# Optimization experiments

Measured on AMD Instinct MI355X. Metric: run time of the kernel, lower is better.

The kernel has to match this reference:

```python
import jax, jax.numpy as jnp
import numpy as np
import math

MSG_K = 256  # min(active_count, 256); with uniform(0,1) activations active_count >> 256
N_HEADS = 4
LN_EPS = 1e-5


def _mha(x, wi, bi, wo, bo):
    # torch nn.MultiheadAttention self-attention, batch_first=True
    B, K, D = x.shape
    H = N_HEADS
    hd = D // H
    qkv = x @ wi.T + bi                      # [B,K,3D]
    q, k, v = jnp.split(qkv, 3, axis=-1)
    def split_heads(t):
        return t.reshape(B, K, H, hd).transpose(0, 2, 1, 3)  # [B,H,K,hd]
    q, k, v = split_heads(q), split_heads(k), split_heads(v)
    scores = jnp.einsum('bhqd,bhkd->bhqk', q, k) * (1.0 / math.sqrt(hd))
    attn = jax.nn.softmax(scores, axis=-1)
    o = jnp.einsum('bhqk,bhkd->bhqd', attn, v)
    o = o.transpose(0, 2, 1, 3).reshape(B, K, D)
    return o @ wo.T + bo


def _layernorm(x, g, b):
    mu = jnp.mean(x, axis=-1, keepdims=True)
    var = jnp.mean((x - mu) ** 2, axis=-1, keepdims=True)
    return (x - mu) * jax.lax.rsqrt(var + LN_EPS) * g + b


def setup_inputs() -> dict:
    key = jax.random.key(0)
    ks = jax.random.split(key, 12)
    B, N, D = 32, 4096, 256
    s = 0.02
    return {
        'activation': jax.random.uniform(ks[0], (B, N), dtype=jnp.float32),
        'hidden_state': jax.random.normal(ks[1], (B, N, D), dtype=jnp.float32),
        'in_proj_w': jax.random.normal(ks[2], (3 * D, D), dtype=jnp.float32) * s,
        'in_proj_b': jnp.zeros((3 * D,), jnp.float32),
        'out_proj_w': jax.random.normal(ks[3], (D, D), dtype=jnp.float32) * s,
        'out_proj_b': jnp.zeros((D,), jnp.float32),
        'su_w1': jax.random.normal(ks[4], (D, 2 * D), dtype=jnp.float32) * s,
        'su_b1': jnp.zeros((D,), jnp.float32),
        'su_w2': jax.random.normal(ks[5], (D, D), dtype=jnp.float32) * s,
        'su_b2': jnp.zeros((D,), jnp.float32),
        'au_w1': jax.random.normal(ks[6], (D, 2 * D), dtype=jnp.float32) * s,
        'au_b1': jnp.zeros((D,), jnp.float32),
        'au_w2': jax.random.normal(ks[7], (1, D), dtype=jnp.float32) * s,
        'au_b2': jnp.zeros((1,), jnp.float32),
        'ln_g': jnp.ones((D,), jnp.float32),
        'ln_b': jnp.zeros((D,), jnp.float32),
        'sparsity_k': 256,
    }


def reference(activation, hidden_state, in_proj_w, in_proj_b, out_proj_w, out_proj_b,
              su_w1, su_b1, su_w2, su_b2, au_w1, au_b1, au_w2, au_b2, ln_g, ln_b,
              sparsity_k):
    B, N, D = hidden_state.shape
    b_idx = jnp.arange(B)[:, None]

    # ---- compute_messages: top-k gather -> sparse MHA -> scatter back ----
    topk_vals, topk_idx = jax.lax.top_k(activation, MSG_K)        # [B,K]
    active_states = jnp.take_along_axis(hidden_state, topk_idx[..., None], axis=1)  # [B,K,D]
    msg_sparse = _mha(active_states, in_proj_w, in_proj_b, out_proj_w, out_proj_b)
    msg_sparse = msg_sparse * topk_vals[..., None]
    messages = jnp.zeros((B, N, D), hidden_state.dtype).at[b_idx, topk_idx].set(msg_sparse)

    # ---- update_states: MLP on [old, messages] + LayerNorm ----
    combined = jnp.concatenate([hidden_state, messages], axis=-1)  # [B,N,2D]
    h = jax.nn.gelu(combined @ su_w1.T + su_b1, approximate=False)
    new_hidden = _layernorm(h @ su_w2.T + su_b2, ln_g, ln_b)

    # ---- update_activations ----
    comb2 = jnp.concatenate([hidden_state, new_hidden], axis=-1)
    h2 = jax.nn.gelu(comb2 @ au_w1.T + au_b1, approximate=False)
    delta = jax.nn.sigmoid((h2 @ au_w2.T + au_b2).squeeze(-1))     # [B,N]
    new_activation = jnp.clip(0.7 * activation + 0.3 * delta, 0.0, 1.0)

    # ---- maintain_sparsity: keep top sparsity_k, zero the rest ----
    k = min(int(sparsity_k), N)
    tv, ti = jax.lax.top_k(new_activation, k)                      # [B,k]
    sparse_act = jnp.zeros_like(new_activation).at[b_idx, ti].set(tv)
    kept_hidden = jnp.take_along_axis(new_hidden, ti[..., None], axis=1)
    sparse_hidden = jnp.zeros_like(new_hidden).at[b_idx, ti].set(kept_hidden)
    return sparse_act, sparse_hidden
```

## Files before the change

kernel.cpp:

```cpp
#include <hip/hip_runtime.h>


constexpr int KC = 32;
constexpr int CMAX = 2304;
constexpr float BAND_EPS = 0.004f;
constexpr int MAXBAND = 512;

typedef short bf16x8 __attribute__((ext_vector_type(8)));
typedef float f32x4 __attribute__((ext_vector_type(4)));

__device__ __forceinline__ float gelu_f(float x) {
    return 0.5f * x * (1.0f + erff(x * 0.70710678118654752440f));
}
__device__ __forceinline__ unsigned short f2bf(float f) {
    unsigned u = __float_as_uint(f);
    return (unsigned short)((u + 0x7fffu + ((u >> 16) & 1u)) >> 16);
}
__device__ __forceinline__ float bf2f(unsigned short h) {
    return __uint_as_float(((unsigned)h) << 16);
}
__device__ __forceinline__ int swz(int row, int byteInRow) {
    return (row << 9) + (byteInRow ^ ((row & 7) << 4));
}

__global__ void __launch_bounds__(256) fill0_k(float4* p, long n4) {
    long i = (long)blockIdx.x * 256 + threadIdx.x;
    long stride = (long)gridDim.x * 256;
    float4 z = make_float4(0.f, 0.f, 0.f, 0.f);
    for (; i < n4; i += stride) p[i] = z;
}

__global__ void __launch_bounds__(256) topk1_k(const float* __restrict__ act,
        float* __restrict__ svals, int* __restrict__ sidx, int* __restrict__ cnt)
{
    __shared__ int cs[4];
    __shared__ int sTop, sRest;
    int b = blockIdx.x, tid = threadIdx.x;
    int wid = tid >> 6, lane = tid & 63;
    unsigned v[16];
    #pragma unroll
    for (int s = 0; s < 16; ++s)
        v[s] = __float_as_uint(act[b * 4096 + s * 256 + tid]);

    auto reduce4 = [&](int c) -> int {
        #pragma unroll
        for (int off = 32; off >= 1; off >>= 1) c += __shfl_xor(c, off);
        if (lane == 0) cs[wid] = c;
        __syncthreads();
        int tot = cs[0] + cs[1] + cs[2] + cs[3];
        __syncthreads();
        return tot;
    };
    auto countGE = [&](unsigned thr) -> int {
        int c = 0;
        #pragma unroll
        for (int s = 0; s < 16; ++s) c += (v[s] >= thr) ? 1 : 0;
        return reduce4(c);
    };
    auto countEqLt = [&](unsigned vs, int icut) -> int {
        int c = 0;
        #pragma unroll
        for (int s = 0; s < 16; ++s)
            c += (v[s] == vs && (s * 256 + tid) < icut) ? 1 : 0;
        return reduce4(c);
    };

    unsigned vstar = 0;
    for (int bit = 31; bit >= 0; --bit) {
        unsigned cand = vstar | (1u << bit);
        if (countGE(cand) >= 256) vstar = cand;
    }
    int cgt = countGE(vstar + 1);
    int needed = 256 - cgt;
    int icut = 4096;
    if (countEqLt(vstar, 4096) > needed) {
        int lo = 0, hi = 4096;
        for (int it = 0; it < 12; ++it) {
            int mid = (lo + hi) >> 1;
            if (countEqLt(vstar, mid) <= needed) lo = mid; else hi = mid;
        }
        icut = lo;
    }
    if (tid == 0) { sTop = 0; sRest = 0; }
    __syncthreads();
    float th = __uint_as_float(vstar) - 0.4288f;
    #pragma unroll
    for (int s = 0; s < 16; ++s) {
        int i = s * 256 + tid;
        unsigned vb = v[s];
        float f = __uint_as_float(vb);
        bool top = (vb > vstar) || (vb == vstar && i < icut);
        if (top) {
            int slot = atomicAdd(&sTop, 1);
            sidx[b * 4096 + slot] = i;
            svals[b * 4096 + slot] = f;
        } else if (f >= th) {
            int slot = 256 + atomicAdd(&sRest, 1);
            if (slot < CMAX) {
                sidx[b * 4096 + slot] = i;
                svals[b * 4096 + slot] = f;
            }
        }
    }
    __syncthreads();
    if (tid == 0) cnt[b] = min(256 + sRest, CMAX);
}

__global__ void __launch_bounds__(256) topk2_k(const float* __restrict__ newact,
        const int* __restrict__ sidx, const int* __restrict__ cnt,
        float* __restrict__ selv, int* __restrict__ selo, int* __restrict__ selp)
{
    __shared__ int cs[4];
    __shared__ int sSel;
    int b = blockIdx.x, tid = threadIdx.x;
    int wid = tid >> 6, lane = tid & 63;
    int C = min(cnt[b], CMAX);
    unsigned v[9];
    int org[9];
    #pragma unroll
    for (int s = 0; s < 9; ++s) {
        int p = s * 256 + tid;
        bool ok = (p < C && p < CMAX);
        v[s] = ok ? __float_as_uint(newact[(long)b * CMAX + p]) : 0u;
        org[s] = ok ? sidx[b * 4096 + p] : 0x7FFFFFFF;
    }
    auto reduce4 = [&](int c) -> int {
        #pragma unroll
        for (int off = 32; off >= 1; off >>= 1) c += __shfl_xor(c, off);
        if (lane == 0) cs[wid] = c;
        __syncthreads();
        int tot = cs[0] + cs[1] + cs[2] + cs[3];
        __syncthreads();
        return tot;
    };
    auto countGE = [&](unsigned thr) -> int {
        int c = 0;
        #pragma unroll
        for (int s = 0; s < 9; ++s) c += (v[s] >= thr) ? 1 : 0;
        return reduce4(c);
    };
    auto countEqLt = [&](unsigned vs, int icut) -> int {
        int c = 0;
        #pragma unroll
        for (int s = 0; s < 9; ++s) c += (v[s] == vs && org[s] < icut) ? 1 : 0;
        return reduce4(c);
    };

    unsigned vstar = 0;
    for (int bit = 31; bit >= 0; --bit) {
        unsigned cand = vstar | (1u << bit);
        if (countGE(cand) >= 256) vstar = cand;
    }
    int cgt = countGE(vstar + 1);
    int needed = 256 - cgt;
    int icut = 4096;
    if (countEqLt(vstar, 4096) > needed) {
        int lo = 0, hi = 4096;
        for (int it = 0; it < 12; ++it) {
            int mid = (lo + hi) >> 1;
            if (countEqLt(vstar, mid) <= needed) lo = mid; else hi = mid;
        }
        icut = lo;
    }
    if (tid == 0) sSel = 0;
    __syncthreads();
    #pragma unroll
    for (int s = 0; s < 9; ++s) {
        unsigned vb = v[s];
        bool sel = (vb > vstar) || (vb == vstar && org[s] < icut);
        if (sel) {
            int slot = atomicAdd(&sSel, 1);
            selv[b * 256 + slot] = __uint_as_float(vb);
            selo[b * 256 + slot] = org[s];
            selp[b * 256 + slot] = s * 256 + tid;
        }
    }
}

template<int TM, int TN, int RM, int RN, bool BT, bool GATHER, int EPI>
__global__ void __launch_bounds__(256) gemm_k(
    const float* __restrict__ A, int lda, long sA1, long sA2, int divA,
    const float* __restrict__ B, int ldb, long sB1, long sB2, int divB,
    float* __restrict__ C, int ldc, long sC1, long sC2, int divC,
    int K, const float* __restrict__ bias, const float* __restrict__ rowscale,
    long rsStride, const int* __restrict__ gmap, long gmapStride, float cscale)
{
    constexpr int TX = TN / RN, TY = TM / RM;
    static_assert(TX * TY == 256, "block must be 256 threads");
    static_assert(EPI != 4 || TX == 32, "softmax epilogue needs TX==32");
    __shared__ float As[KC][TM + 4];
    __shared__ float Bs[KC][TN + 4];
    int z = blockIdx.z;
    const float* Ab = A + (long)(z / divA) * sA1 + (long)(z % divA) * sA2;
    const float* Bb = B + (long)(z / divB) * sB1 + (long)(z % divB) * sB2;
    float* Cb = C + (long)(z / divC) * sC1 + (long)(z % divC) * sC2;
    int m0 = blockIdx.y * TM, n0 = blockIdx.x * TN;
    int tid = threadIdx.x;
    int tx = tid % TX, ty = tid / TX;
    float acc[RM][RN];
    #pragma unroll
    for (int i = 0; i < RM; ++i)
        #pragma unroll
        for (int j = 0; j < RN; ++j) acc[i][j] = 0.f;

    for (int k0 = 0; k0 < K; k0 += KC) {
        __syncthreads();
        #pragma unroll
        for (int u = 0; u < (TM * KC) / 1024; ++u) {
            int idx = tid + u * 256;
            int m = idx / (KC / 4), k4 = idx % (KC / 4);
            int row = m0 + m;
            long grow = GATHER ? (long)gmap[(long)z * gmapStride + row] : (long)row;
            float4 v = *(const float4*)(Ab + grow * lda + k0 + k4 * 4);
            As[k4 * 4 + 0][m] = v.x; As[k4 * 4 + 1][m] = v.y;
            As[k4 * 4 + 2][m] = v.z; As[k4 * 4 + 3][m] = v.w;
        }
        if (BT) {
            #pragma unroll
            for (int u = 0; u < (TN * KC) / 1024; ++u) {
                int idx = tid + u * 256;
                int n = idx / (KC / 4), k4 = idx % (KC / 4);
                float4 v = *(const float4*)(Bb + (long)(n0 + n) * ldb + k0 + k4 * 4);
                Bs[k4 * 4 + 0][n] = v.x; Bs[k4 * 4 + 1][n] = v.y;
                Bs[k4 * 4 + 2][n] = v.z; Bs[k4 * 4 + 3][n] = v.w;
            }
        } else {
            #pragma unroll
            for (int u = 0; u < (TN * KC) / 1024; ++u) {
                int idx = tid + u * 256;
                int k = idx / (TN / 4), n4 = idx % (TN / 4);
                float4 v = *(const float4*)(Bb + (long)(k0 + k) * ldb + n0 + n4 * 4);
                *(float4*)&Bs[k][n4 * 4] = v;
            }
        }
        __syncthreads();
        #pragma unroll
        for (int k = 0; k < KC; ++k) {
            float av[RM], bv[RN];
            #pragma unroll
            for (int i = 0; i < RM; i += 4) {
                float4 t = *(const float4*)&As[k][ty * RM + i];
                av[i] = t.x; av[i + 1] = t.y; av[i + 2] = t.z; av[i + 3] = t.w;
            }
            #pragma unroll
            for (int j = 0; j < RN; j += 4) {
                float4 t = *(const float4*)&Bs[k][tx * RN + j];
                bv[j] = t.x; bv[j + 1] = t.y; bv[j + 2] = t.z; bv[j + 3] = t.w;
            }
            #pragma unroll
            for (int i = 0; i < RM; ++i)
                #pragma unroll
                for (int j = 0; j < RN; ++j)
                    acc[i][j] = fmaf(av[i], bv[j], acc[i][j]);
        }
    }
    if (EPI == 4) {
        #pragma unroll
        for (int i = 0; i < RM; ++i) {
            float m = -1e30f;
            #pragma unroll
            for (int j = 0; j < RN; ++j) {
                acc[i][j] *= cscale;
                m = fmaxf(m, acc[i][j]);
            }
            #pragma unroll
            for (int off = 16; off >= 1; off >>= 1) m = fmaxf(m, __shfl_xor(m, off));
            float s = 0.f;
            #pragma unroll
            for (int j = 0; j < RN; ++j) {
                acc[i][j] = expf(acc[i][j] - m);
                s += acc[i][j];
            }
            #pragma unroll
            for (int off = 16; off >= 1; off >>= 1) s += __shfl_xor(s, off);
            float inv = 1.f / s;
            #pragma unroll
            for (int j = 0; j < RN; ++j) acc[i][j] *= inv;
        }
    }
    #pragma unroll
    for (int i = 0; i < RM; ++i) {
        int gm = m0 + ty * RM + i;
        float rs = 1.f;
        if (EPI == 2) rs = rowscale[(long)z * rsStride + gm];
        #pragma unroll
        for (int j = 0; j < RN; j += 4) {
            int gn = n0 + tx * RN + j;
            float4 v = make_float4(acc[i][j], acc[i][j + 1], acc[i][j + 2], acc[i][j + 3]);
            if (EPI == 1 || EPI == 2) {
                float4 bb = *(const float4*)(bias + gn);
                v.x += bb.x; v.y += bb.y; v.z += bb.z; v.w += bb.w;
            }
            if (EPI == 2) { v.x *= rs; v.y *= rs; v.z *= rs; v.w *= rs; }
            if (EPI == 3) { v.x *= cscale; v.y *= cscale; v.z *= cscale; v.w *= cscale; }
            *(float4*)(Cb + (long)gm * ldc + gn) = v;
        }
    }
}

__global__ void __launch_bounds__(256) msgc_k(
    const float* __restrict__ Ob,
    const float* __restrict__ wo,
    const float* __restrict__ bo,
    const float* __restrict__ su_w1,
    const float* __restrict__ svals,
    float* __restrict__ MSGC)
{
    constexpr int TM = 32, TN = 256, RM = 4, RN = 8;
    constexpr int TX = TN / RN;
    __shared__ float As[KC][TM + 4];
    __shared__ float Bs[KC][TN + 4];
    __shared__ float Ms[TM][TN + 4];
    int b = blockIdx.y;
    int m0 = blockIdx.x * TM;
    int tid = threadIdx.x;
    int tx = tid % TX, ty = tid / TX;
    const float* Ab = Ob + (long)b * 65536;
    float acc[RM][RN];

    #pragma unroll
    for (int i = 0; i < RM; ++i)
        #pragma unroll
        for (int j = 0; j < RN; ++j) acc[i][j] = 0.f;
    for (int k0 = 0; k0 < 256; k0 += KC) {
        __syncthreads();
        {
            int m = tid / (KC / 4), k4 = tid % (KC / 4);
            float4 v = *(const float4*)(Ab + (long)(m0 + m) * 256 + k0 + k4 * 4);
            As[k4 * 4 + 0][m] = v.x; As[k4 * 4 + 1][m] = v.y;
            As[k4 * 4 + 2][m] = v.z; As[k4 * 4 + 3][m] = v.w;
        }
        #pragma unroll
        for (int u = 0; u < 8; ++u) {
            int idx = tid + u * 256;
            int n = idx / (KC / 4), k4 = idx % (KC / 4);
            float4 v = *(const float4*)(wo + (long)n * 256 + k0 + k4 * 4);
            Bs[k4 * 4 + 0][n] = v.x; Bs[k4 * 4 + 1][n] = v.y;
            Bs[k4 * 4 + 2][n] = v.z; Bs[k4 * 4 + 3][n] = v.w;
        }
        __syncthreads();
        #pragma unroll
        for (int k = 0; k < KC; ++k) {
            float av[RM], bv[RN];
            float4 ta = *(const float4*)&As[k][ty * RM];
            av[0] = ta.x; av[1] = ta.y; av[2] = ta.z; av[3] = ta.w;
            #pragma unroll
            for (int j = 0; j < RN; j += 4) {
                float4 t = *(const float4*)&Bs[k][tx * RN + j];
                bv[j] = t.x; bv[j + 1] = t.y; bv[j + 2] = t.z; bv[j + 3] = t.w;
            }
            #pragma unroll
            for (int i = 0; i < RM; ++i)
                #pragma unroll
                for (int j = 0; j < RN; ++j)
                    acc[i][j] = fmaf(av[i], bv[j], acc[i][j]);
        }
    }
    __syncthreads();
    #pragma unroll
    for (int i = 0; i < RM; ++i) {
        int gm = m0 + ty * RM + i;
        float tv = svals[b * 4096 + gm];
        #pragma unroll
        for (int j = 0; j < RN; j += 4) {
            int gn = tx * RN + j;
            float4 bb = *(const float4*)(bo + gn);
            float4 v;
            v.x = (acc[i][j + 0] + bb.x) * tv;
            v.y = (acc[i][j + 1] + bb.y) * tv;
            v.z = (acc[i][j + 2] + bb.z) * tv;
            v.w = (acc[i][j + 3] + bb.w) * tv;
            *(float4*)&Ms[ty * RM + i][gn] = v;
        }
    }

    #pragma unroll
    for (int i = 0; i < RM; ++i)
        #pragma unroll
        for (int j = 0; j < RN; ++j) acc[i][j] = 0.f;
    const float* W1b = su_w1 + 256;
    for (int k0 = 0; k0 < 256; k0 += KC) {
        __syncthreads();
        #pragma unroll
        for (int u = 0; u < 8; ++u) {
            int idx = tid + u * 256;
            int n = idx / (KC / 4), k4 = idx % (KC / 4);
            float4 v = *(const float4*)(W1b + (long)n * 512 + k0 + k4 * 4);
            Bs[k4 * 4 + 0][n] = v.x; Bs[k4 * 4 + 1][n] = v.y;
            Bs[k4 * 4 + 2][n] = v.z; Bs[k4 * 4 + 3][n] = v.w;
        }
        __syncthreads();
        #pragma unroll
        for (int k = 0; k < KC; ++k) {
            float av[RM], bv[RN];
            #pragma unroll
            for (int i = 0; i < RM; ++i)
                av[i] = Ms[ty * RM + i][k0 + k];
            #pragma unroll
            for (int j = 0; j < RN; j += 4) {
                float4 t = *(const float4*)&Bs[k][tx * RN + j];
                bv[j] = t.x; bv[j + 1] = t.y; bv[j + 2] = t.z; bv[j + 3] = t.w;
            }
            #pragma unroll
            for (int i = 0; i < RM; ++i)
                #pragma unroll
                for (int j = 0; j < RN; ++j)
                    acc[i][j] = fmaf(av[i], bv[j], acc[i][j]);
        }
    }
    float* Cb = MSGC + (long)b * 65536;
    #pragma unroll
    for (int i = 0; i < RM; ++i) {
        int gm = m0 + ty * RM + i;
        #pragma unroll
        for (int j = 0; j < RN; j += 4) {
            int gn = tx * RN + j;
            float4 v = make_float4(acc[i][j], acc[i][j + 1], acc[i][j + 2], acc[i][j + 3]);
            *(float4*)(Cb + (long)gm * 256 + gn) = v;
        }
    }
}

__global__ void __launch_bounds__(256) prep_k(
        const float* __restrict__ s1, const float* __restrict__ s2,
        const float* __restrict__ a1,
        unsigned short* __restrict__ o1, unsigned short* __restrict__ o2,
        unsigned short* __restrict__ o3,
        float* __restrict__ w1P, float* __restrict__ w2P, float* __restrict__ auP)
{
    int blk = blockIdx.x, tid = threadIdx.x;
    if (blk < 512) {
        int i = blk * 256 + tid;
        o1[i] = f2bf(s1[i]);
        o3[i] = f2bf(a1[i]);
        if (i < 65536) o2[i] = f2bf(s2[i]);
        return;
    }
    const float* src; float* dst; int ld, ktiles, rel;
    if (blk < 576) { rel = blk - 512; src = s1; ld = 512; dst = w1P; ktiles = 8; }
    else if (blk < 640) { rel = blk - 576; src = s2; ld = 256; dst = w2P; ktiles = 8; }
    else { rel = blk - 640; src = a1; ld = 512; dst = auP; ktiles = 16; }
    int k0 = (rel % ktiles) * 32, n0 = (rel / ktiles) * 32;
    __shared__ float t[32][33];
    int tx = tid & 31, ty = tid >> 5;
    #pragma unroll
    for (int yy = 0; yy < 4; ++yy) {
        int nl = ty * 4 + yy;
        t[nl][tx] = src[(long)(n0 + nl) * ld + k0 + tx];
    }
    __syncthreads();
    #pragma unroll
    for (int yy = 0; yy < 4; ++yy) {
        int k = k0 + ty * 4 + yy;
        dst[(long)(k >> 2) * 1024 + (n0 + tx) * 4 + (k & 3)] = t[tx][ty * 4 + yy];
    }
}

__global__ void __launch_bounds__(256) gatherX_k(const float* __restrict__ hid,
        const int* __restrict__ sidx, const int* __restrict__ cnt,
        unsigned short* __restrict__ Xb)
{
    int b = blockIdx.y;
    int C = min(cnt[b], CMAX);
    int p = blockIdx.x * 4 + (threadIdx.x >> 6);
    int lane = threadIdx.x & 63;
    unsigned short* dst = Xb + ((long)b * CMAX + p) * 256 + lane * 4;
    if (p < C) {
        int row = sidx[b * 4096 + p];
        float4 v = *(const float4*)(hid + ((long)b * 4096 + row) * 256 + lane * 4);
        ushort4 o; o.x = f2bf(v.x); o.y = f2bf(v.y); o.z = f2bf(v.z); o.w = f2bf(v.w);
        *(ushort4*)dst = o;
    } else {
        ushort4 z; z.x = 0; z.y = 0; z.z = 0; z.w = 0;
        *(ushort4*)dst = z;
    }
}

__global__ void __launch_bounds__(256, 2) fused_mlp_k(
    const unsigned short* __restrict__ Xb,
    const unsigned short* __restrict__ W1,
    const unsigned short* __restrict__ W2,
    const unsigned short* __restrict__ WA,
    const float* __restrict__ su_b1v, const float* __restrict__ msgc,
    const float* __restrict__ su_b2v,
    const float* __restrict__ lng, const float* __restrict__ lnb,
    const float* __restrict__ au_b1v,
    const float* __restrict__ w2v, const float* __restrict__ b2s,
    const float* __restrict__ svals, const int* __restrict__ cnt,
    unsigned short* __restrict__ NHb, float* __restrict__ nac)
{
    int b = blockIdx.y;
    int C = min(cnt[b], CMAX);
    int m0 = blockIdx.x * 64;
    if (m0 >= C) return;
    int tid = threadIdx.x;
    int wid = tid >> 6;
    int lane = tid & 63;
    int l15 = lane & 15;
    int q = lane >> 4;
    int n0w = wid * 64;

    __shared__ __align__(16) unsigned short Xs[64 * 256];
    __shared__ __align__(16) unsigned short Hs[64 * 256];
    __shared__ float rsum[4][64];
    __shared__ float rsq[4][64];
    __shared__ float rmu[64], rrs[64];

    const unsigned short* Ab = Xb + ((long)b * CMAX + m0) * 256;

    #pragma unroll
    for (int rnd = 0; rnd < 8; ++rnd) {
        int idx = rnd * 256 + tid;
        int r = idx >> 5, c = idx & 31;
        bf16x8 v = *(const bf16x8*)(Ab + r * 256 + c * 8);
        *(bf16x8*)((char*)Xs + swz(r, c * 16)) = v;
    }
    __syncthreads();

    f32x4 acc[4][4];

    #pragma unroll
    for (int mt = 0; mt < 4; ++mt)
        #pragma unroll
        for (int nt = 0; nt < 4; ++nt) {
            f32x4 z = {0.f, 0.f, 0.f, 0.f};
            acc[mt][nt] = z;
        }
    {
        const unsigned short* wr[4];
        #pragma unroll
        for (int nt = 0; nt < 4; ++nt) wr[nt] = W1 + (long)(n0w + nt * 16 + l15) * 512;
        #pragma unroll 4
        for (int ks = 0; ks < 8; ++ks) {
            int ko = ks * 32;
            bf16x8 af[4], bfr[4];
            #pragma unroll
            for (int mt = 0; mt < 4; ++mt)
                af[mt] = *(const bf16x8*)((const char*)Xs +
                         swz(mt * 16 + l15, (ko + q * 8) * 2));
            #pragma unroll
            for (int nt = 0; nt < 4; ++nt)
                bfr[nt] = *(const bf16x8*)(wr[nt] + ko + q * 8);
            #pragma unroll
            for (int mt = 0; mt < 4; ++mt)
                #pragma unroll
                for (int nt = 0; nt < 4; ++nt)
                    acc[mt][nt] = __builtin_amdgcn_mfma_f32_16x16x32_bf16(
                        af[mt], bfr[nt], acc[mt][nt], 0, 0, 0);
        }
        float bb[4];
        #pragma unroll
        for (int nt = 0; nt < 4; ++nt) bb[nt] = su_b1v[n0w + nt * 16 + l15];
        #pragma unroll
        for (int mt = 0; mt < 4; ++mt) {
            #pragma unroll
            for (int reg = 0; reg < 4; ++reg) {
                int lr = mt * 16 + q * 4 + reg;
                int p = m0 + lr;
                const float* mrow = msgc + ((long)b * 256 + p) * 256;
                bool hasm = (p < 256);
                #pragma unroll
                for (int nt = 0; nt < 4; ++nt) {
                    int gc = n0w + nt * 16 + l15;
                    float v = acc[mt][nt][reg] + bb[nt];
                    if (hasm) v += mrow[gc];
                    *(unsigned short*)((char*)Hs + swz(lr, gc * 2)) = f2bf(gelu_f(v));
                }
            }
        }
    }
    __syncthreads();

    #pragma unroll
    for (int mt = 0; mt < 4; ++mt)
        #pragma unroll
        for (int nt = 0; nt < 4; ++nt) {
            f32x4 z = {0.f, 0.f, 0.f, 0.f};
            acc[mt][nt] = z;
        }
    {
        const unsigned short* wr[4];
        #pragma unroll
        for (int nt = 0; nt < 4; ++nt) wr[nt] = W2 + (long)(n0w + nt * 16 + l15) * 256;
        #pragma unroll
        for (int ks = 0; ks < 8; ++ks) {
            int ko = ks * 32;
            bf16x8 af[4], bfr[4];
            #pragma unroll
            for (int mt = 0; mt < 4; ++mt) {
                int r = mt * 16 + l15;
                af[mt] = *(const bf16x8*)((const char*)Hs + swz(r, (ko + q * 8) * 2));
            }
            #pragma unroll
            for (int nt = 0; nt < 4; ++nt)
                bfr[nt] = *(const bf16x8*)(wr[nt] + ko + q * 8);
            #pragma unroll
            for (int mt = 0; mt < 4; ++mt)
                #pragma unroll
                for (int nt = 0; nt < 4; ++nt)
                    acc[mt][nt] = __builtin_amdgcn_mfma_f32_16x16x32_bf16(
                        af[mt], bfr[nt], acc[mt][nt], 0, 0, 0);
        }
        float bb[4], gg[4], eb[4];
        #pragma unroll
        for (int nt = 0; nt < 4; ++nt) {
            int gc = n0w + nt * 16 + l15;
            bb[nt] = su_b2v[gc]; gg[nt] = lng[gc]; eb[nt] = lnb[gc];
        }
        #pragma unroll
        for (int mt = 0; mt < 4; ++mt)
            #pragma unroll
            for (int nt = 0; nt < 4; ++nt)
                #pragma unroll
                for (int reg = 0; reg < 4; ++reg)
                    acc[mt][nt][reg] += bb[nt];
        #pragma unroll
        for (int mt = 0; mt < 4; ++mt) {
            #pragma unroll
            for (int reg = 0; reg < 4; ++reg) {
                float s = 0.f, s2 = 0.f;
                #pragma unroll
                for (int nt = 0; nt < 4; ++nt) {
                    float v = acc[mt][nt][reg];
                    s += v; s2 += v * v;
                }
                #pragma unroll
                for (int off = 1; off <= 8; off <<= 1) {
                    s += __shfl_xor(s, off);
                    s2 += __shfl_xor(s2, off);
                }
                if (l15 == 0) {
                    int row = mt * 16 + q * 4 + reg;
                    rsum[wid][row] = s; rsq[wid][row] = s2;
                }
            }
        }
        __syncthreads();
        if (tid < 64) {
            float s = rsum[0][tid] + rsum[1][tid] + rsum[2][tid] + rsum[3][tid];
            float s2 = rsq[0][tid] + rsq[1][tid] + rsq[2][tid] + rsq[3][tid];
            float mu = s * (1.f / 256.f);
            float var = s2 * (1.f / 256.f) - mu * mu;
            rmu[tid] = mu;
            rrs[tid] = rsqrtf(var + 1e-5f);
        }
        __syncthreads();
        #pragma unroll
        for (int mt = 0; mt < 4; ++mt) {
            #pragma unroll
            for (int reg = 0; reg < 4; ++reg) {
                int lr = mt * 16 + q * 4 + reg;
                float mu = rmu[lr], rs = rrs[lr];
                #pragma unroll
                for (int nt = 0; nt < 4; ++nt) {
                    int gc = n0w + nt * 16 + l15;
                    unsigned short ov =
                        f2bf((acc[mt][nt][reg] - mu) * rs * gg[nt] + eb[nt]);
                    *(unsigned short*)((char*)Hs + swz(lr, gc * 2)) = ov;
                }
            }
        }
    }
    __syncthreads();

    #pragma unroll
    for (int rnd = 0; rnd < 8; ++rnd) {
        int idx = rnd * 256 + tid;
        int r = idx >> 5, c = idx & 31;
        bf16x8 v = *(const bf16x8*)((const char*)Hs + swz(r, c * 16));
        *(bf16x8*)(NHb + ((long)b * CMAX + m0 + r) * 256 + c * 8) = v;
    }

    #pragma unroll
    for (int mt = 0; mt < 4; ++mt)
        #pragma unroll
        for (int nt = 0; nt < 4; ++nt) {
            f32x4 z = {0.f, 0.f, 0.f, 0.f};
            acc[mt][nt] = z;
        }
    {
        const unsigned short* wr[4];
        #pragma unroll
        for (int nt = 0; nt < 4; ++nt) wr[nt] = WA + (long)(n0w + nt * 16 + l15) * 512;
        #pragma unroll 4
        for (int ks = 0; ks < 8; ++ks) {
            int ko = ks * 32;
            bf16x8 af[4], bfr[4];
            #pragma unroll
            for (int mt = 0; mt < 4; ++mt)
                af[mt] = *(const bf16x8*)((const char*)Xs +
                         swz(mt * 16 + l15, (ko + q * 8) * 2));
            #pragma unroll
            for (int nt = 0; nt < 4; ++nt)
                bfr[nt] = *(const bf16x8*)(wr[nt] + ko + q * 8);
            #pragma unroll
            for (int mt = 0; mt < 4; ++mt)
                #pragma unroll
                for (int nt = 0; nt < 4; ++nt)
                    acc[mt][nt] = __builtin_amdgcn_mfma_f32_16x16x32_bf16(
                        af[mt], bfr[nt], acc[mt][nt], 0, 0, 0);
        }
        #pragma unroll
        for (int ks = 0; ks < 8; ++ks) {
            int ko = ks * 32;
            int kw = 256 + ks * 32;
            bf16x8 af[4], bfr[4];
            #pragma unroll
            for (int mt = 0; mt < 4; ++mt) {
                int r = mt * 16 + l15;
                af[mt] = *(const bf16x8*)((const char*)Hs + swz(r, (ko + q * 8) * 2));
            }
            #pragma unroll
            for (int nt = 0; nt < 4; ++nt)
                bfr[nt] = *(const bf16x8*)(wr[nt] + kw + q * 8);
            #pragma unroll
            for (int mt = 0; mt < 4; ++mt)
                #pragma unroll
                for (int nt = 0; nt < 4; ++nt)
                    acc[mt][nt] = __builtin_amdgcn_mfma_f32_16x16x32_bf16(
                        af[mt], bfr[nt], acc[mt][nt], 0, 0, 0);
        }
        float bb[4], ww[4];
        #pragma unroll
        for (int nt = 0; nt < 4; ++nt) {
            int gc = n0w + nt * 16 + l15;
            bb[nt] = au_b1v[gc]; ww[nt] = w2v[gc];
        }
        #pragma unroll
        for (int mt = 0; mt < 4; ++mt) {
            #pragma unroll
            for (int reg = 0; reg < 4; ++reg) {
                float s = 0.f;
                #pragma unroll
                for (int nt = 0; nt < 4; ++nt)
                    s += gelu_f(acc[mt][nt][reg] + bb[nt]) * ww[nt];
                #pragma unroll
                for (int off = 1; off <= 8; off <<= 1) s += __shfl_xor(s, off);
                if (l15 == 0) rsum[wid][mt * 16 + q * 4 + reg] = s;
            }
        }
        __syncthreads();
        if (tid < 64) {
            int p = m0 + tid;
            if (p < C) {
                float z = rsum[0][tid] + rsum[1][tid] + rsum[2][tid] + rsum[3][tid] + b2s[0];
                float delta = 1.f / (1.f + expf(-z));
                float na = 0.7f * svals[b * 4096 + p] + 0.3f * delta;
                nac[(long)b * CMAX + p] = fminf(fmaxf(na, 0.f), 1.f);
            }
        }
    }
}

__global__ void __launch_bounds__(256) selectT_k(const float* __restrict__ nac,
        const int* __restrict__ cnt, float* __restrict__ T)
{
    __shared__ float v[CMAX];
    __shared__ int cs[4];
    int b = blockIdx.x, tid = threadIdx.x;
    int wid = tid >> 6, lane = tid & 63;
    int C = min(cnt[b], CMAX);
    for (int i = tid; i < CMAX; i += 256)
        v[i] = (i < C) ? nac[(long)b * CMAX + i] : -1.f;
    __syncthreads();
    float lo = 0.f, hi = 1.f;
    for (int it = 0; it < 20; ++it) {
        float mid = 0.5f * (lo + hi);
        int c = 0;
        for (int i = tid; i < CMAX; i += 256) c += (v[i] >= mid) ? 1 : 0;
        #pragma unroll
        for (int off = 32; off >= 1; off >>= 1) c += __shfl_xor(c, off);
        if (lane == 0) cs[wid] = c;
        __syncthreads();
        int tot = cs[0] + cs[1] + cs[2] + cs[3];
        __syncthreads();
        if (tot >= 256) lo = mid; else hi = mid;
    }
    if (tid == 0) T[b] = lo;
}

__global__ void __launch_bounds__(256) bandlist_k(const float* __restrict__ nac,
        const int* __restrict__ cnt, const float* __restrict__ Tarr,
        int* __restrict__ bandlist, int* __restrict__ bandcnt)
{
    int b = blockIdx.y;
    int C = min(cnt[b], CMAX);
    int p = blockIdx.x * 256 + threadIdx.x;
    if (p < C && fabsf(nac[(long)b * CMAX + p] - Tarr[b]) < BAND_EPS) {
        int slot = atomicAdd(&bandcnt[b], 1);
        if (slot < MAXBAND) bandlist[b * MAXBAND + slot] = p;
    }
}

__global__ void __launch_bounds__(256) bandfix_k(
    const float* __restrict__ hid, const int* __restrict__ sidx,
    const float* __restrict__ msgc,
    const float* __restrict__ w1Pf, const float* __restrict__ su_b1,
    const float* __restrict__ w2Pf, const float* __restrict__ su_b2,
    const float* __restrict__ ln_g, const float* __restrict__ ln_b,
    const float* __restrict__ auPf, const float* __restrict__ au_b1,
    const float* __restrict__ au_w2, const float* __restrict__ au_b2,
    const float* __restrict__ svals,
    const int* __restrict__ bandlist, const int* __restrict__ bandcnt,
    float* __restrict__ nac, unsigned short* __restrict__ NHb)
{
    int b = blockIdx.y;
    int M = min(bandcnt[b], MAXBAND);
    int base = blockIdx.x * 4;
    if (base >= M) return;
    int nact = min(M - base, 4);
    int tid = threadIdx.x;
    int wid = tid >> 6, lane = tid & 63;
    const float4* w1P = (const float4*)w1Pf;
    const float4* w2P = (const float4*)w2Pf;
    const float4* auP = (const float4*)auPf;
    __shared__ float xr[4][256];
    __shared__ float hy[4][256];
    __shared__ float nh[4][256];
    __shared__ float muS[4], rsS[4];
    __shared__ int ppS[4];
    if (tid < 4)
        ppS[tid] = (tid < nact) ? bandlist[b * MAXBAND + base + tid] : -1;
    __syncthreads();
    #pragma unroll
    for (int r = 0; r < 4; ++r) {
        int pp = ppS[r];
        xr[r][tid] = (pp >= 0) ? hid[((long)b * 4096 + sidx[b * 4096 + pp]) * 256 + tid] : 0.f;
    }
    __syncthreads();
    int n = tid;
    float acc[4];
    #pragma unroll
    for (int r = 0; r < 4; ++r) acc[r] = 0.f;
    for (int k4 = 0; k4 < 64; ++k4) {
        float4 w = w1P[k4 * 256 + n];
        #pragma unroll
        for (int r = 0; r < 4; ++r) {
            float4 xv = *(const float4*)&xr[r][k4 * 4];
            acc[r] = fmaf(w.x, xv.x, acc[r]);
            acc[r] = fmaf(w.y, xv.y, acc[r]);
            acc[r] = fmaf(w.z, xv.z, acc[r]);
            acc[r] = fmaf(w.w, xv.w, acc[r]);
        }
    }
    float b1v = su_b1[n];
    #pragma unroll
    for (int r = 0; r < 4; ++r) {
        int pp = ppS[r];
        float s = acc[r] + b1v;
        if (pp >= 0 && pp < 256) s += msgc[((long)b * 256 + pp) * 256 + n];
        acc[r] = gelu_f(s);
    }
    __syncthreads();
    #pragma unroll
    for (int r = 0; r < 4; ++r) hy[r][n] = acc[r];
    __syncthreads();
    #pragma unroll
    for (int r = 0; r < 4; ++r) acc[r] = 0.f;
    for (int k4 = 0; k4 < 64; ++k4) {
        float4 w = w2P[k4 * 256 + n];
        #pragma unroll
        for (int r = 0; r < 4; ++r) {
            float4 hv = *(const float4*)&hy[r][k4 * 4];
            acc[r] = fmaf(w.x, hv.x, acc[r]);
            acc[r] = fmaf(w.y, hv.y, acc[r]);
            acc[r] = fmaf(w.z, hv.z, acc[r]);
            acc[r] = fmaf(w.w, hv.w, acc[r]);
        }
    }
    __syncthreads();
    float b2v = su_b2[n];
    #pragma unroll
    for (int r = 0; r < 4; ++r) hy[r][n] = acc[r] + b2v;
    __syncthreads();
    {
        int r = wid;
        float4 yv = *(const float4*)&hy[r][lane * 4];
        float s = yv.x + yv.y + yv.z + yv.w;
        float s2 = yv.x * yv.x + yv.y * yv.y + yv.z * yv.z + yv.w * yv.w;
        #pragma unroll
        for (int off = 32; off >= 1; off >>= 1) {
            s += __shfl_xor(s, off);
            s2 += __shfl_xor(s2, off);
        }
        if (lane == 0) {
            float mu = s * (1.f / 256.f);
            float var = s2 * (1.f / 256.f) - mu * mu;
            muS[r] = mu; rsS[r] = rsqrtf(var + 1e-5f);
        }
    }
    __syncthreads();
    float gv = ln_g[n], ev = ln_b[n];
    #pragma unroll
    for (int r = 0; r < 4; ++r) {
        float o = (hy[r][n] - muS[r]) * rsS[r] * gv + ev;
        nh[r][n] = o;
        if (ppS[r] >= 0) NHb[((long)b * CMAX + ppS[r]) * 256 + n] = f2bf(o);
    }
    __syncthreads();
    #pragma unroll
    for (int r = 0; r < 4; ++r) acc[r] = 0.f;
    for (int k4 = 0; k4 < 64; ++k4) {
        float4 w = auP[k4 * 256 + n];
        #pragma unroll
        for (int r = 0; r < 4; ++r) {
            float4 xv = *(const float4*)&xr[r][k4 * 4];
            acc[r] = fmaf(w.x, xv.x, acc[r]);
            acc[r] = fmaf(w.y, xv.y, acc[r]);
            acc[r] = fmaf(w.z, xv.z, acc[r]);
            acc[r] = fmaf(w.w, xv.w, acc[r]);
        }
    }
    for (int k4 = 64; k4 < 128; ++k4) {
        float4 w = auP[k4 * 256 + n];
        #pragma unroll
        for (int r = 0; r < 4; ++r) {
            float4 hv = *(const float4*)&nh[r][(k4 - 64) * 4];
            acc[r] = fmaf(w.x, hv.x, acc[r]);
            acc[r] = fmaf(w.y, hv.y, acc[r]);
            acc[r] = fmaf(w.z, hv.z, acc[r]);
            acc[r] = fmaf(w.w, hv.w, acc[r]);
        }
    }
    float ab = au_b1[n], wv2 = au_w2[n];
    __syncthreads();
    #pragma unroll
    for (int r = 0; r < 4; ++r) hy[r][n] = gelu_f(acc[r] + ab) * wv2;
    __syncthreads();
    {
        int r = wid;
        float4 gvv = *(const float4*)&hy[r][lane * 4];
        float s = gvv.x + gvv.y + gvv.z + gvv.w;
        #pragma unroll
        for (int off = 32; off >= 1; off >>= 1) s += __shfl_xor(s, off);
        if (lane == 0 && ppS[r] >= 0) {
            float z = s + au_b2[0];
            float delta = 1.f / (1.f + expf(-z));
            float na = 0.7f * svals[b * 4096 + ppS[r]] + 0.3f * delta;
            nac[(long)b * CMAX + ppS[r]] = fminf(fmaxf(na, 0.f), 1.f);
        }
    }
}

__global__ void __launch_bounds__(64) scatter_k(const float* __restrict__ selv,
        const int* __restrict__ selo, const int* __restrict__ selp,
        const unsigned short* __restrict__ NHb, float* __restrict__ out)
{
    int b = blockIdx.x >> 8, j = blockIdx.x & 255, t = threadIdx.x;
    int orig = selo[b * 256 + j];
    int p = selp[b * 256 + j];
    if (t == 0) out[b * 4096 + orig] = selv[b * 256 + j];
    const ushort4* src = (const ushort4*)(NHb + ((long)b * CMAX + p) * 256);
    ushort4 s = src[t];
    float4 o = make_float4(bf2f(s.x), bf2f(s.y), bf2f(s.z), bf2f(s.w));
    *(float4*)(out + 131072 + ((long)(b * 4096 + orig)) * 256 + t * 4) = o;
}

extern "C" void kernel_launch(void* const* d_in, const int* in_sizes, int n_in,
                              void* d_out, int out_size, void* d_ws, size_t ws_size,
                              hipStream_t stream)
{
    const float* act   = (const float*)d_in[0];
    const float* hid   = (const float*)d_in[1];
    const float* wi    = (const float*)d_in[2];
    const float* bi    = (const float*)d_in[3];
    const float* wo    = (const float*)d_in[4];
    const float* bo    = (const float*)d_in[5];
    const float* su_w1 = (const float*)d_in[6];
    const float* su_b1 = (const float*)d_in[7];
    const float* su_w2 = (const float*)d_in[8];
    const float* su_b2 = (const float*)d_in[9];
    const float* au_w1 = (const float*)d_in[10];
    const float* au_b1 = (const float*)d_in[11];
    const float* au_w2 = (const float*)d_in[12];
    const float* au_b2 = (const float*)d_in[13];
    const float* ln_g  = (const float*)d_in[14];
    const float* ln_b  = (const float*)d_in[15];
    float* out = (float*)d_out;

    char* ws = (char*)d_ws;
    size_t off = 0;
    auto alloc = [&](size_t bytes) {
        size_t o = off; off += (bytes + 255) & ~(size_t)255; return o;
    };
    float* svals = (float*)(ws + alloc((size_t)32 * 4096 * 4));
    int*   sidx  = (int*)  (ws + alloc((size_t)32 * 4096 * 4));
    int*   cnt   = (int*)  (ws + alloc(256));
    float* qkv   = (float*)(ws + alloc((size_t)32 * 256 * 768 * 4));
    float* Sb    = (float*)(ws + alloc((size_t)32 * 4 * 256 * 256 * 4));
    float* Ob    = (float*)(ws + alloc((size_t)32 * 256 * 256 * 4));
    float* MSGC  = (float*)(ws + alloc((size_t)32 * 256 * 256 * 4));
    float* selv  = (float*)(ws + alloc((size_t)32 * 256 * 4));
    int*   selo  = (int*)  (ws + alloc((size_t)32 * 256 * 4));
    int*   selp  = (int*)  (ws + alloc((size_t)32 * 256 * 4));
    unsigned short* swb1 = (unsigned short*)(ws + alloc((size_t)256 * 512 * 2));
    unsigned short* swb2 = (unsigned short*)(ws + alloc((size_t)256 * 256 * 2));
    unsigned short* awb1 = (unsigned short*)(ws + alloc((size_t)256 * 512 * 2));
    float* w1P = (float*)(ws + alloc((size_t)256 * 256 * 4));
    float* w2P = (float*)(ws + alloc((size_t)256 * 256 * 4));
    float* auP = (float*)(ws + alloc((size_t)512 * 256 * 4));
    unsigned short* Xb   = (unsigned short*)(ws + alloc((size_t)32 * CMAX * 256 * 2));
    unsigned short* NHb  = (unsigned short*)(ws + alloc((size_t)32 * CMAX * 256 * 2));
    float* nac = (float*)(ws + alloc((size_t)32 * CMAX * 4));
    float* Tb  = (float*)(ws + alloc(128));
    int* bandl = (int*)(ws + alloc((size_t)32 * MAXBAND * 4));
    int* bandc = (int*)(ws + alloc(128));

    hipMemsetAsync(bandc, 0, 32 * sizeof(int), stream);
    fill0_k<<<2048, 256, 0, stream>>>((float4*)out, (long)out_size / 4);
    topk1_k<<<32, 256, 0, stream>>>(act, svals, sidx, cnt);
    prep_k<<<768, 256, 0, stream>>>(su_w1, su_w2, au_w1, swb1, swb2, awb1,
                                    w1P, w2P, auP);
    gatherX_k<<<dim3(CMAX / 4, 32), 256, 0, stream>>>(hid, sidx, cnt, Xb);
    gemm_k<64, 256, 8, 8, true, true, 1><<<dim3(3, 4, 32), 256, 0, stream>>>(
        hid, 256, (long)4096 * 256, 0, 1,
        wi, 256, 0, 0, 1,
        qkv, 768, (long)256 * 768, 0, 1,
        256, bi, nullptr, 0, sidx, 4096, 0.f);
    gemm_k<64, 256, 8, 8, true, false, 4><<<dim3(1, 4, 128), 256, 0, stream>>>(
        qkv, 768, 196608, 64, 4,
        qkv + 256, 768, 196608, 64, 4,
        Sb, 256, 65536, 0, 1,
        64, nullptr, nullptr, 0, nullptr, 0, 0.125f);
    gemm_k<64, 64, 4, 4, false, false, 0><<<dim3(1, 4, 128), 256, 0, stream>>>(
        Sb, 256, 65536, 0, 1,
        qkv + 512, 768, 196608, 64, 4,
        Ob, 256, 65536, 64, 4,
        256, nullptr, nullptr, 0, nullptr, 0, 0.f);
    msgc_k<<<dim3(8, 32), 256, 0, stream>>>(Ob, wo, bo, su_w1, svals, MSGC);
    fused_mlp_k<<<dim3(CMAX / 64, 32), 256, 0, stream>>>(Xb, swb1, swb2, awb1,
        su_b1, MSGC, su_b2, ln_g, ln_b, au_b1, au_w2, au_b2, svals, cnt,
        NHb, nac);
    selectT_k<<<32, 256, 0, stream>>>(nac, cnt, Tb);
    bandlist_k<<<dim3(CMAX / 256, 32), 256, 0, stream>>>(nac, cnt, Tb, bandl, bandc);
    bandfix_k<<<dim3(MAXBAND / 4, 32), 256, 0, stream>>>(hid, sidx, MSGC,
        w1P, su_b1, w2P, su_b2, ln_g, ln_b, auP, au_b1, au_w2, au_b2,
        svals, bandl, bandc, nac, NHb);
    topk2_k<<<32, 256, 0, stream>>>(nac, sidx, cnt, selv, selo, selp);
    scatter_k<<<8192, 64, 0, stream>>>(selv, selo, selp, NHb, out);
}
```

Baseline: 690.0 us.

## Fuse QK^T, softmax and PV into one attention kernel; deterministic top-k compaction

Replaces the two attention GEMM launches with a single attention kernel. Each block computes a 32-query tile's scores in shared memory, applies softmax and multiplies by V, so the 32MB score buffer is never written to or read from global memory. The top-k compaction in topk1 now uses a wave prefix scan with packed counters instead of shared-memory atomics. This makes slot order deterministic but adds barriers per iteration. The attention grid grows to 1024 blocks with a large shared footprint, about 75KB, which may limit occupancy.

```diff
diff --git a/kernel.cpp b/kernel.cpp
--- a/kernel.cpp
+++ b/kernel.cpp
@@ -34,7 +34,6 @@
         float* __restrict__ svals, int* __restrict__ sidx, int* __restrict__ cnt)
 {
     __shared__ int cs[4];
-    __shared__ int sTop, sRest;
     int b = blockIdx.x, tid = threadIdx.x;
     int wid = tid >> 6, lane = tid & 63;
     unsigned v[16];
@@ -81,29 +80,43 @@
         }
         icut = lo;
     }
-    if (tid == 0) { sTop = 0; sRest = 0; }
-    __syncthreads();
     float th = __uint_as_float(vstar) - 0.4288f;
-    #pragma unroll
+    int basePacked = 0;
     for (int s = 0; s < 16; ++s) {
         int i = s * 256 + tid;
         unsigned vb = v[s];
         float f = __uint_as_float(vb);
         bool top = (vb > vstar) || (vb == vstar && i < icut);
+        bool rest = (!top) && (f >= th);
+        int flag = (top ? 1 : 0) | (rest ? (1 << 16) : 0);
+        int x = flag;
+        #pragma unroll
+        for (int off = 1; off < 64; off <<= 1) {
+            int n = __shfl_up(x, off);
+            if (lane >= off) x += n;
+        }
+        if (lane == 63) cs[wid] = x;
+        __syncthreads();
+        int waveOff = 0;
+        #pragma unroll
+        for (int w = 0; w < 4; ++w) if (w < wid) waveOff += cs[w];
+        int tot = cs[0] + cs[1] + cs[2] + cs[3];
+        int excl = x - flag + waveOff;
         if (top) {
-            int slot = atomicAdd(&sTop, 1);
+            int slot = (basePacked & 0xffff) + (excl & 0xffff);
             sidx[b * 4096 + slot] = i;
             svals[b * 4096 + slot] = f;
-        } else if (f >= th) {
-            int slot = 256 + atomicAdd(&sRest, 1);
+        } else if (rest) {
+            int slot = 256 + (basePacked >> 16) + (excl >> 16);
             if (slot < CMAX) {
                 sidx[b * 4096 + slot] = i;
                 svals[b * 4096 + slot] = f;
             }
         }
-    }
-    __syncthreads();
-    if (tid == 0) cnt[b] = min(256 + sRest, CMAX);
+        basePacked += tot;
+        __syncthreads();
+    }
+    if (tid == 0) cnt[b] = min(256 + (basePacked >> 16), CMAX);
 }
 
 __global__ void __launch_bounds__(256) topk2_k(const float* __restrict__ newact,
@@ -187,7 +200,6 @@
 {
     constexpr int TX = TN / RN, TY = TM / RM;
     static_assert(TX * TY == 256, "block must be 256 threads");
-    static_assert(EPI != 4 || TX == 32, "softmax epilogue needs TX==32");
     __shared__ float As[KC][TM + 4];
     __shared__ float Bs[KC][TN + 4];
     int z = blockIdx.z;
@@ -254,30 +266,6 @@
                     acc[i][j] = fmaf(av[i], bv[j], acc[i][j]);
         }
     }
-    if (EPI == 4) {
-        #pragma unroll
-        for (int i = 0; i < RM; ++i) {
-            float m = -1e30f;
-            #pragma unroll
-            for (int j = 0; j < RN; ++j) {
-                acc[i][j] *= cscale;
-                m = fmaxf(m, acc[i][j]);
-            }
-            #pragma unroll
-            for (int off = 16; off >= 1; off >>= 1) m = fmaxf(m, __shfl_xor(m, off));
-            float s = 0.f;
-            #pragma unroll
-            for (int j = 0; j < RN; ++j) {
-                acc[i][j] = expf(acc[i][j] - m);
-                s += acc[i][j];
-            }
-            #pragma unroll
-            for (int off = 16; off >= 1; off >>= 1) s += __shfl_xor(s, off);
-            float inv = 1.f / s;
-            #pragma unroll
-            for (int j = 0; j < RN; ++j) acc[i][j] *= inv;
-        }
-    }
     #pragma unroll
     for (int i = 0; i < RM; ++i) {
         int gm = m0 + ty * RM + i;
@@ -294,6 +282,132 @@
             if (EPI == 2) { v.x *= rs; v.y *= rs; v.z *= rs; v.w *= rs; }
             if (EPI == 3) { v.x *= cscale; v.y *= cscale; v.z *= cscale; v.w *= cscale; }
             *(float4*)(Cb + (long)gm * ldc + gn) = v;
+        }
+    }
+}
+
+__global__ void __launch_bounds__(256) attn_k(
+    const float* __restrict__ qkv, float* __restrict__ Ob)
+{
+    __shared__ float As[32][68];
+    __shared__ float Bs[32][260];
+    __shared__ float Ss[32][260];
+    int qt = blockIdx.x, h = blockIdx.y, b = blockIdx.z;
+    int tid = threadIdx.x;
+    const float* Qb = qkv + (long)b * 196608 + h * 64;
+    const float* Kb = Qb + 256;
+    const float* Vb = Qb + 512;
+    int m0 = qt * 32;
+
+    {
+        int tx = tid & 31, ty = tid >> 5;
+        float acc[4][8];
+        #pragma unroll
+        for (int i = 0; i < 4; ++i)
+            #pragma unroll
+            for (int j = 0; j < 8; ++j) acc[i][j] = 0.f;
+        for (int k0 = 0; k0 < 64; k0 += 32) {
+            __syncthreads();
+            {
+                int m = tid >> 3, k4 = tid & 7;
+                float4 v = *(const float4*)(Qb + (long)(m0 + m) * 768 + k0 + k4 * 4);
+                As[k4 * 4 + 0][m] = v.x; As[k4 * 4 + 1][m] = v.y;
+                As[k4 * 4 + 2][m] = v.z; As[k4 * 4 + 3][m] = v.w;
+            }
+            #pragma unroll
+            for (int u = 0; u < 8; ++u) {
+                int idx = tid + u * 256;
+                int n = idx >> 3, k4 = idx & 7;
+                float4 v = *(const float4*)(Kb + (long)n * 768 + k0 + k4 * 4);
+                Bs[k4 * 4 + 0][n] = v.x; Bs[k4 * 4 + 1][n] = v.y;
+                Bs[k4 * 4 + 2][n] = v.z; Bs[k4 * 4 + 3][n] = v.w;
+            }
+            __syncthreads();
+            #pragma unroll
+            for (int k = 0; k < 32; ++k) {
+                float av[4], bv[8];
+                float4 ta = *(const float4*)&As[k][ty * 4];
+                av[0] = ta.x; av[1] = ta.y; av[2] = ta.z; av[3] = ta.w;
+                #pragma unroll
+                for (int j = 0; j < 8; j += 4) {
+                    float4 t = *(const float4*)&Bs[k][tx * 8 + j];
+                    bv[j] = t.x; bv[j + 1] = t.y; bv[j + 2] = t.z; bv[j + 3] = t.w;
+                }
+                #pragma unroll
+                for (int i = 0; i < 4; ++i)
+                    #pragma unroll
+                    for (int j = 0; j < 8; ++j)
+                        acc[i][j] = fmaf(av[i], bv[j], acc[i][j]);
+            }
+        }
+        #pragma unroll
+        for (int i = 0; i < 4; ++i) {
+            float m = -1e30f;
+            #pragma unroll
+            for (int j = 0; j < 8; ++j) {
+                acc[i][j] *= 0.125f;
+                m = fmaxf(m, acc[i][j]);
+            }
+            #pragma unroll
+            for (int off = 16; off >= 1; off >>= 1) m = fmaxf(m, __shfl_xor(m, off));
+            float s = 0.f;
+            #pragma unroll
+            for (int j = 0; j < 8; ++j) {
+                acc[i][j] = expf(acc[i][j] - m);
+                s += acc[i][j];
+            }
+            #pragma unroll
+            for (int off = 16; off >= 1; off >>= 1) s += __shfl_xor(s, off);
+            float inv = 1.f / s;
+            #pragma unroll
+            for (int j = 0; j < 8; ++j) acc[i][j] *= inv;
+        }
+        #pragma unroll
+        for (int i = 0; i < 4; ++i)
+            #pragma unroll
+            for (int j = 0; j < 8; j += 4) {
+                float4 v = make_float4(acc[i][j], acc[i][j + 1],
+                                       acc[i][j + 2], acc[i][j + 3]);
+                *(float4*)&Ss[ty * 4 + i][tx * 8 + j] = v;
+            }
+    }
+    {
+        int tx = tid & 15, ty = tid >> 4;
+        float acc[2][4];
+        #pragma unroll
+        for (int i = 0; i < 2; ++i)
+            #pragma unroll
+            for (int j = 0; j < 4; ++j) acc[i][j] = 0.f;
+        for (int k0 = 0; k0 < 256; k0 += 32) {
+            __syncthreads();
+            #pragma unroll
+            for (int u = 0; u < 2; ++u) {
+                int idx = tid + u * 256;
+                int k = idx >> 4, n4 = idx & 15;
+                float4 v = *(const float4*)(Vb + (long)(k0 + k) * 768 + n4 * 4);
+                *(float4*)&As[k][n4 * 4] = v;
+            }
+            __syncthreads();
+            #pragma unroll
+            for (int k = 0; k < 32; ++k) {
+                float av[2], bv[4];
+                av[0] = Ss[ty * 2 + 0][k0 + k];
+                av[1] = Ss[ty * 2 + 1][k0 + k];
+                float4 t = *(const float4*)&As[k][tx * 4];
+                bv[0] = t.x; bv[1] = t.y; bv[2] = t.z; bv[3] = t.w;
+                #pragma unroll
+                for (int i = 0; i < 2; ++i)
+                    #pragma unroll
+                    for (int j = 0; j < 4; ++j)
+                        acc[i][j] = fmaf(av[i], bv[j], acc[i][j]);
+            }
+        }
+        float* Cb = Ob + (long)b * 65536 + h * 64;
+        #pragma unroll
+        for (int i = 0; i < 2; ++i) {
+            int gm = m0 + ty * 2 + i;
+            float4 v = make_float4(acc[i][0], acc[i][1], acc[i][2], acc[i][3]);
+            *(float4*)(Cb + (long)gm * 256 + tx * 4) = v;
         }
     }
 }
@@ -987,7 +1101,6 @@
     int*   sidx  = (int*)  (ws + alloc((size_t)32 * 4096 * 4));
     int*   cnt   = (int*)  (ws + alloc(256));
     float* qkv   = (float*)(ws + alloc((size_t)32 * 256 * 768 * 4));
-    float* Sb    = (float*)(ws + alloc((size_t)32 * 4 * 256 * 256 * 4));
     float* Ob    = (float*)(ws + alloc((size_t)32 * 256 * 256 * 4));
     float* MSGC  = (float*)(ws + alloc((size_t)32 * 256 * 256 * 4));
     float* selv  = (float*)(ws + alloc((size_t)32 * 256 * 4));
@@ -1017,16 +1130,7 @@
         wi, 256, 0, 0, 1,
         qkv, 768, (long)256 * 768, 0, 1,
         256, bi, nullptr, 0, sidx, 4096, 0.f);
-    gemm_k<64, 256, 8, 8, true, false, 4><<<dim3(1, 4, 128), 256, 0, stream>>>(
-        qkv, 768, 196608, 64, 4,
-        qkv + 256, 768, 196608, 64, 4,
-        Sb, 256, 65536, 0, 1,
-        64, nullptr, nullptr, 0, nullptr, 0, 0.125f);
-    gemm_k<64, 64, 4, 4, false, false, 0><<<dim3(1, 4, 128), 256, 0, stream>>>(
-        Sb, 256, 65536, 0, 1,
-        qkv + 512, 768, 196608, 64, 4,
-        Ob, 256, 65536, 64, 4,
-        256, nullptr, nullptr, 0, nullptr, 0, 0.f);
+    attn_k<<<dim3(8, 4, 32), 256, 0, stream>>>(qkv, Ob);
     msgc_k<<<dim3(8, 32), 256, 0, stream>>>(Ob, wo, bo, su_w1, svals, MSGC);
     fused_mlp_k<<<dim3(CMAX / 64, 32), 256, 0, stream>>>(Xb, swb1, swb2, awb1,
         su_b1, MSGC, su_b2, ln_g, ln_b, au_b1, au_w2, au_b2, svals, cnt,
```

Result: slower. 718.0 us (+4.1%).
